# Kernel tuning notes

Measured on AMD Instinct MI355X. Metric: run time of the kernel, lower is better.

Reference implementation:

```python
import jax, jax.numpy as jnp
import numpy as np

D_MODEL = 1024
D_STATE = 64
D_CONV = 4
EXPAND = 2
N_HEADS = 16
D_INNER = D_MODEL * EXPAND            # 2048
HEAD_DIM = D_INNER // N_HEADS         # 128
Z_DIM = D_INNER + 2 * D_STATE * N_HEADS + N_HEADS  # 4112
RMS_EPS = 1.1920928955078125e-07      # torch.finfo(float32).eps (RMSNorm default)


def setup_inputs() -> dict:
    key = jax.random.key(0)
    ks = jax.random.split(key, 6)
    s = 0.02
    u = jax.random.normal(ks[0], (2, 4096, D_MODEL), dtype=jnp.float32)
    W_in = jax.random.normal(ks[1], (D_MODEL, Z_DIM), dtype=jnp.float32) * s
    conv_w = jax.random.normal(ks[2], (D_INNER, D_CONV), dtype=jnp.float32) * s
    conv_b = jnp.zeros((D_INNER,), dtype=jnp.float32)
    delta_param = jnp.zeros((N_HEADS,), dtype=jnp.float32)
    W_gate = jax.random.normal(ks[3], (D_MODEL, D_INNER), dtype=jnp.float32) * s
    norm_w = jnp.ones((D_INNER,), dtype=jnp.float32)
    W_out = jax.random.normal(ks[4], (D_INNER, D_MODEL), dtype=jnp.float32) * s
    return {"u": u, "W_in": W_in, "conv_w": conv_w, "conv_b": conv_b,
            "delta_param": delta_param, "W_gate": W_gate, "norm_w": norm_w, "W_out": W_out}


def _ssm_scan(x, dt, B_mat, C_mat, delta_param):
    # x: (B,L,nh,dh); dt: (B,L,nh); B_mat,C_mat: (B,L,nh,ds)
    delta = jax.nn.softplus(dt + delta_param[None, None, :])
    a_bar = jnp.exp(-delta * jnp.abs(dt))            # (B,L,nh)
    Bsz, L, nh, dh = x.shape
    ds = B_mat.shape[-1]
    h0 = jnp.zeros((Bsz, nh, dh, ds), dtype=x.dtype)

    def step(h, inp):
        a_t, x_t, b_t, c_t = inp                     # (B,nh),(B,nh,dh),(B,nh,ds),(B,nh,ds)
        h = a_t[:, :, None, None] * h + x_t[..., None] * b_t[:, :, None, :]
        y_t = jnp.einsum('bhds,bhs->bhd', h, c_t)
        return h, y_t

    # move time to leading axis for scan
    xs = (jnp.moveaxis(a_bar, 1, 0), jnp.moveaxis(x, 1, 0),
          jnp.moveaxis(B_mat, 1, 0), jnp.moveaxis(C_mat, 1, 0))
    _, ys = jax.lax.scan(step, h0, xs)               # ys: (L,B,nh,dh)
    return jnp.moveaxis(ys, 0, 1)                    # (B,L,nh,dh)


def _forward(u, W_in, conv_w, conv_b, delta_param, W_gate, norm_w, W_out):
    B, L, _ = u.shape
    z = u @ W_in                                      # (B,L,Z_DIM)
    x = z[..., :D_INNER]
    o = D_INNER
    B_mat = z[..., o:o + D_STATE * N_HEADS].reshape(B, L, N_HEADS, D_STATE)
    o += D_STATE * N_HEADS
    C_mat = z[..., o:o + D_STATE * N_HEADS].reshape(B, L, N_HEADS, D_STATE)
    o += D_STATE * N_HEADS
    dt = z[..., o:o + N_HEADS]                        # (B,L,nh)

    # depthwise causal conv1d (kernel size D_CONV, left pad D_CONV-1)
    pad = D_CONV - 1
    xp = jnp.pad(x, ((0, 0), (pad, 0), (0, 0)))       # (B,L+pad,d_inner)
    x_conv = conv_b[None, None, :]
    for k in range(D_CONV):
        x_conv = x_conv + xp[:, k:k + L, :] * conv_w[None, None, :, k]
    x = jax.nn.silu(x_conv)

    x_ssm = x.reshape(B, L, N_HEADS, HEAD_DIM)
    y = _ssm_scan(x_ssm, dt, B_mat, C_mat, delta_param)
    y = y.reshape(B, L, D_INNER)

    gate = jax.nn.sigmoid(u @ W_gate)
    y = gate * y
    # RMSNorm
    y = y * jax.lax.rsqrt(jnp.mean(y * y, axis=-1, keepdims=True) + RMS_EPS) * norm_w
    return y @ W_out


def reference(u, W_in, conv_w, conv_b, delta_param, W_gate, norm_w, W_out):
    return _forward(u, W_in, conv_w, conv_b, delta_param, W_gate, norm_w, W_out)
```

## Files before the change

kernel.cpp:

```cpp
#include <hip/hip_runtime.h>

#define BATCH   2
#define LSEQ    4096
#define DMODEL  1024
#define DINNER  2048
#define NHEADS  16
#define DSTATE  64
#define HEADDIM 128
#define ZDIM    4112
#define BLROWS  (BATCH*LSEQ)
#define QCHUNK  64
#define NCHUNK  (LSEQ/QCHUNK)
#define UPAD    1088
#define GPAD    2112

#define AS1 __attribute__((address_space(1)))
#define AS3 __attribute__((address_space(3)))

typedef __bf16 bf16;
typedef __bf16 bf16x8 __attribute__((ext_vector_type(8)));
typedef __bf16 bf16x4 __attribute__((ext_vector_type(4)));
typedef float  f32x4  __attribute__((ext_vector_type(4)));

__device__ __forceinline__ int lds_elem(int row, int c)
{
    return (row >> 1) * 64 + (row & 1) * 32 + (((c ^ ((row >> 1) & 3)) & 3) << 3);
}

__global__ void cvt_pad_kernel(const float* __restrict__ in, bf16* __restrict__ out)
{
    int gid = blockIdx.x * 256 + threadIdx.x;
    int row = gid >> 8, c4 = (gid & 255) * 4;
    float4 v = *reinterpret_cast<const float4*>(in + (size_t)row * DMODEL + c4);
    bf16x4 o;
    o[0] = (bf16)v.x; o[1] = (bf16)v.y; o[2] = (bf16)v.z; o[3] = (bf16)v.w;
    *reinterpret_cast<bf16x4*>(out + (size_t)row * UPAD + c4) = o;
}

__global__ void transpose_cvt_kernel(const float* __restrict__ src, bf16* __restrict__ dst,
                                     int R, int C, int Cpad, int dstS,
                                     const float* __restrict__ rowscale)
{
    __shared__ float tile[32][33];
    int tx = threadIdx.x;
    int ty = threadIdx.y;
    int c0 = blockIdx.x * 32;
    int r0 = blockIdx.y * 32;
#pragma unroll
    for (int q = 0; q < 4; q++) {
        int r = r0 + ty + q * 8;
        int c = c0 + tx;
        float v = 0.f;
        if (r < R && c < C) v = src[(size_t)r * C + c];
        tile[ty + q * 8][tx] = v;
    }
    __syncthreads();
    float sc = 1.f;
    if (rowscale && (r0 + tx) < R) sc = rowscale[r0 + tx];
#pragma unroll
    for (int q = 0; q < 4; q++) {
        int oc = c0 + ty + q * 8;
        int orr = r0 + tx;
        if (oc < Cpad && orr < R)
            dst[(size_t)oc * dstS + orr] = (bf16)(tile[tx][ty + q * 8] * sc);
    }
}

template<int NSLICE, int KROW, int MODE, int NBN>
__global__ __launch_bounds__(256) void gemm_db3_kernel(
    const bf16* __restrict__ A, const bf16* __restrict__ Bt,
    bf16* __restrict__ z, bf16* __restrict__ g, float* __restrict__ lab,
    const float* __restrict__ dparam, const float* __restrict__ rs, float* __restrict__ c32)
{
    constexpr int SLOTSZ = 256 * 32;
    __shared__ __align__(16) bf16 lds[3 * SLOTSZ];
    const int tid = threadIdx.x;
    const int lane = tid & 63, wid = tid >> 6;
    const int wm = (wid >> 1) * 64, wn = (wid & 1) * 64;
    const int lml = lane & 15, kc = lane >> 4;

    const int bid = blockIdx.x;
    const int xcd = bid & 7;
    const int idx = bid >> 3;
    const int bm = xcd * 8 + (idx & 7);
    const int bn = idx >> 3;

    const bf16* Abase = A + (size_t)(bm * 128) * KROW;
    const bf16* Bbase = Bt + (size_t)(bn * 128) * KROW;

#define STAGE8(pp) do {                                                                  \
    const int _p = (pp); const int _slot = _p % 3; const size_t _ko = (size_t)_p * 32;   \
    _Pragma("unroll") for (int it = 0; it < 4; ++it) {                                   \
        int q = it * 256 + tid;                                                          \
        int o = (q < 512) ? q : q - 512;                                                 \
        int prow = o >> 3, wi = o & 7;                                                   \
        int row = prow * 2 + (wi >> 2), c = (wi & 3) ^ (prow & 3);                       \
        const bf16* _src = ((q < 512) ? Abase : Bbase) + (size_t)row * KROW + _ko + c * 8; \
        int _dst = _slot * SLOTSZ + ((q < 512) ? 0 : 4096) + o * 8;                      \
        __builtin_amdgcn_global_load_lds((const AS1 void*)_src,                          \
            (AS3 void*)(&lds[_dst]), 16, 0, 0);                                          \
    }                                                                                    \
} while (0)

    f32x4 acc[4][4];
#pragma unroll
    for (int i = 0; i < 4; i++)
#pragma unroll
        for (int j = 0; j < 4; j++) acc[i][j] = (f32x4){0.f, 0.f, 0.f, 0.f};

    STAGE8(0); STAGE8(1); STAGE8(2);
    asm volatile("s_waitcnt vmcnt(8)" ::: "memory");
    __builtin_amdgcn_s_barrier();

    for (int p = 0; p < NSLICE; ++p) {
        const bf16* base_ = &lds[(p % 3) * SLOTSZ];
        bf16x8 af[4], bfv[4];
#pragma unroll
        for (int i = 0; i < 4; ++i) {
            int row = wm + i * 16 + lml;
            af[i] = *reinterpret_cast<const bf16x8*>(&base_[lds_elem(row, kc)]);
        }
#pragma unroll
        for (int j = 0; j < 4; ++j) {
            int row = wn + j * 16 + lml;
            bfv[j] = *reinterpret_cast<const bf16x8*>(&base_[4096 + lds_elem(row, kc)]);
        }
        asm volatile("s_waitcnt lgkmcnt(0)" ::: "memory");
        __builtin_amdgcn_sched_barrier(0);
        __builtin_amdgcn_s_barrier();
        if (p + 3 < NSLICE) STAGE8(p + 3);
#pragma unroll
        for (int i = 0; i < 4; ++i)
#pragma unroll
            for (int j = 0; j < 4; ++j)
                acc[i][j] = __builtin_amdgcn_mfma_f32_16x16x32_bf16(af[i], bfv[j], acc[i][j], 0, 0, 0);
        if (p + 1 < NSLICE) {
            if (p + 3 < NSLICE)       { asm volatile("s_waitcnt vmcnt(8)" ::: "memory"); }
            else if (p + 2 < NSLICE)  { asm volatile("s_waitcnt vmcnt(4)" ::: "memory"); }
            else                      { asm volatile("s_waitcnt vmcnt(0)" ::: "memory"); }
            __builtin_amdgcn_s_barrier();
        }
    }
#undef STAGE8

    const int rbase = (lane >> 4) * 4;
#pragma unroll
    for (int i = 0; i < 4; i++) {
#pragma unroll
        for (int j = 0; j < 4; j++) {
            int col = bn * 128 + wn + j * 16 + lml;
            if constexpr (MODE == 0) {
                bool isZ = (col < ZDIM);
                bool isG = (col >= 4224) && (col < 4224 + DINNER);
                bool isDT = (col >= 4096) && (col < ZDIM);
                if (!isZ && !isG) continue;
#pragma unroll
                for (int r = 0; r < 4; r++) {
                    int row = bm * 128 + wm + i * 16 + rbase + r;
                    float v = acc[i][j][r];
                    if (isZ) {
                        z[(size_t)row * ZDIM + col] = (bf16)v;
                        if (isDT) {
                            int h = col - 4096;
                            float v2 = v + dparam[h];
                            float sp = (v2 > 20.f) ? v2 : log1pf(expf(v2));
                            lab[(size_t)row * NHEADS + h] = -sp * fabsf(v);
                        }
                    } else {
                        g[(size_t)row * GPAD + (col - 4224)] = (bf16)v;
                    }
                }
            } else {
                int row0 = bm * 128 + wm + i * 16 + rbase;
                float4 rsv = *reinterpret_cast<const float4*>(rs + row0);
                const float* rp = reinterpret_cast<const float*>(&rsv);
#pragma unroll
                for (int r = 0; r < 4; r++)
                    c32[(size_t)(row0 + r) * 1024 + col] = acc[i][j][r] * rp[r];
            }
        }
    }
}

__global__ __launch_bounds__(256) void chunk_state_kernel(
    const bf16* __restrict__ zz,
    const float* __restrict__ conv_w, const float* __restrict__ conv_b,
    const float* __restrict__ la,
    bf16* __restrict__ S,
    float* __restrict__ Adec)
{
    __shared__ __align__(16) bf16 xt[HEADDIM * QCHUNK];
    __shared__ __align__(16) bf16 bw[DSTATE * QCHUNK];
    __shared__ float Ls[QCHUNK];
    const int blk = blockIdx.x;
    const int h = blk & 15, c = (blk >> 4) & 63, b = blk >> 10;
    const int tid = threadIdx.x, lane = tid & 63, w = tid >> 6;
    const size_t row0 = (size_t)b * LSEQ + (size_t)c * QCHUNK;
    const bf16* zxg = zz + row0 * ZDIM + h * HEADDIM;
    const bf16* Bg  = zz + row0 * ZDIM + DINNER + h * DSTATE;

    const int tg = (tid >> 4) * 4;
    const int dg8 = (tid & 15) * 8;
    float wv[8][4], xa[4][8];
#pragma unroll
    for (int e = 0; e < 8; e++) {
        float4 w4 = *reinterpret_cast<const float4*>(conv_w + (size_t)(h * HEADDIM + dg8 + e) * 4);
        wv[e][0] = w4.x; wv[e][1] = w4.y; wv[e][2] = w4.z; wv[e][3] = w4.w;
        float bb = conv_b[h * HEADDIM + dg8 + e];
#pragma unroll
        for (int tt = 0; tt < 4; tt++) xa[tt][e] = bb;
    }
#pragma unroll
    for (int r = 0; r < 7; r++) {
        int lrow = c * QCHUNK + tg + r - 3;
        if (lrow >= 0) {
            bf16x8 zv = *reinterpret_cast<const bf16x8*>(zxg + (ptrdiff_t)(tg + r - 3) * ZDIM + dg8);
#pragma unroll
            for (int tt = 0; tt < 4; tt++) {
                int k = r - tt;
                if (k >= 0 && k < 4) {
#pragma unroll
                    for (int e = 0; e < 8; e++)
                        xa[tt][e] = fmaf((float)zv[e], wv[e][k], xa[tt][e]);
                }
            }
        }
    }
#pragma unroll
    for (int tt = 0; tt < 4; tt++)
#pragma unroll
        for (int e = 0; e < 8; e++)
            xa[tt][e] = xa[tt][e] / (1.f + expf(-xa[tt][e]));

    const int t = tid >> 2, sseg = (tid & 3) * 16;
    bf16x8 br[2];
#pragma unroll
    for (int q = 0; q < 2; q++)
        br[q] = *reinterpret_cast<const bf16x8*>(Bg + (size_t)t * ZDIM + sseg + q * 8);

    if (w == 0) {
        float v = la[(row0 + lane) * NHEADS + h];
#pragma unroll
        for (int off = 1; off < 64; off <<= 1) { float o = __shfl_up(v, off); if (lane >= off) v += o; }
        Ls[lane] = v;
        if (lane == 63) Adec[((size_t)b * NHEADS + h) * NCHUNK + c] = __expf(v);
    }
    __syncthreads();
    const float wt = __expf(Ls[QCHUNK - 1] - Ls[t]);
#pragma unroll
    for (int tt = 0; tt < 4; tt++) {
        int t2 = tg + tt;
#pragma unroll
        for (int e = 0; e < 8; e++) {
            int d = dg8 + e;
            xt[d * 64 + (((t2 >> 3) ^ (d & 7)) << 3) + (t2 & 7)] = (bf16)xa[tt][e];
        }
    }
    const int tb = t >> 3, ti = t & 7;
#pragma unroll
    for (int q = 0; q < 2; q++)
#pragma unroll
        for (int j = 0; j < 8; j++) {
            int s = sseg + q * 8 + j;
            bw[s * 64 + ((tb ^ (s & 7)) << 3) + ti] = (bf16)((float)br[q][j] * wt);
        }
    __syncthreads();

    f32x4 acc[2][4];
#pragma unroll
    for (int i = 0; i < 2; i++)
#pragma unroll
        for (int j = 0; j < 4; j++) acc[i][j] = (f32x4){0.f, 0.f, 0.f, 0.f};
#pragma unroll
    for (int kk = 0; kk < 2; kk++) {
        const int kb = kk * 4 + (lane >> 4);
        bf16x8 af[2], bf2[4];
#pragma unroll
        for (int i = 0; i < 2; i++) {
            int d = w * 32 + i * 16 + (lane & 15);
            af[i] = *reinterpret_cast<const bf16x8*>(&xt[d * 64 + ((kb ^ (d & 7)) << 3)]);
        }
#pragma unroll
        for (int j = 0; j < 4; j++) {
            int s = j * 16 + (lane & 15);
            bf2[j] = *reinterpret_cast<const bf16x8*>(&bw[s * 64 + ((kb ^ (s & 7)) << 3)]);
        }
#pragma unroll
        for (int i = 0; i < 2; i++)
#pragma unroll
            for (int j = 0; j < 4; j++)
                acc[i][j] = __builtin_amdgcn_mfma_f32_16x16x32_bf16(af[i], bf2[j], acc[i][j], 0, 0, 0);
    }
    bf16* Sg = S + ((size_t)(b * NCHUNK + c) * NHEADS + h) * (HEADDIM * DSTATE);
    const int rr = (lane >> 4) * 4, ccol = lane & 15;
#pragma unroll
    for (int i = 0; i < 2; i++)
#pragma unroll
        for (int j = 0; j < 4; j++)
#pragma unroll
            for (int r = 0; r < 4; r++)
                Sg[(w * 32 + i * 16 + rr + r) * 64 + j * 16 + ccol] = (bf16)acc[i][j][r];
}

__global__ void chunk_carry_kernel(bf16* S, const float* __restrict__ A)
{
    int gid = blockIdx.x * 256 + threadIdx.x;
    if (gid >= BATCH * NHEADS * HEADDIM * DSTATE) return;
    int es = gid & (HEADDIM * DSTATE - 1);
    int h  = (gid >> 13) & (NHEADS - 1);
    int b  = gid >> 17;
    const float* Ab = A + ((size_t)b * NHEADS + h) * NCHUNK;
    float hstate = 0.f;
    size_t stride = (size_t)NHEADS * HEADDIM * DSTATE;
    bf16* p = S + ((size_t)b * NCHUNK * NHEADS + h) * (HEADDIM * DSTATE) + es;
    for (int c = 0; c < NCHUNK; ++c) {
        float sv = (float)*p;
        *p = (bf16)hstate;
        hstate = fmaf(Ab[c], hstate, sv);
        p += stride;
    }
}

__global__ __launch_bounds__(256) void chunk_y_kernel(
    bf16* __restrict__ gv,
    const bf16* __restrict__ zz,
    const float* __restrict__ conv_w, const float* __restrict__ conv_b,
    const float* __restrict__ la,
    const bf16* __restrict__ H,
    float* __restrict__ psum)
{
    __shared__ __align__(16) bf16 bc[QCHUNK * 128];
    __shared__ __align__(16) bf16 xt[HEADDIM * QCHUNK];
    __shared__ __align__(16) bf16 hl[HEADDIM * DSTATE];
    __shared__ float Ls[QCHUNK];
    __shared__ float wsum[4][QCHUNK];
    const int blk = blockIdx.x;
    const int h = blk & 15, c = (blk >> 4) & 63, b = blk >> 10;
    const int tid = threadIdx.x, lane = tid & 63, w = tid >> 6;
    const size_t row0 = (size_t)b * LSEQ + (size_t)c * QCHUNK;
    bf16* gg = gv + row0 * GPAD + h * HEADDIM;
    const bf16* zxg = zz + row0 * ZDIM + h * HEADDIM;
    const bf16* Bg = zz + row0 * ZDIM + DINNER + h * DSTATE;
    const bf16* Cg = Bg + NHEADS * DSTATE;
    const bf16* Hg = H + ((size_t)(b * NCHUNK + c) * NHEADS + h) * (HEADDIM * DSTATE);

#pragma unroll
    for (int it = 0; it < 2; it++) {
        int idx = it * 256 + tid;
        int row = idx >> 3, p = idx & 7;
        int sc = (p ^ (row & 7)) << 3;
        __builtin_amdgcn_global_load_lds((const AS1 void*)(Bg + (size_t)row * ZDIM + sc),
                                         (AS3 void*)(&bc[idx * 8]), 16, 0, 0);
        __builtin_amdgcn_global_load_lds((const AS1 void*)(Cg + (size_t)row * ZDIM + sc),
                                         (AS3 void*)(&bc[4096 + idx * 8]), 16, 0, 0);
    }
#pragma unroll
    for (int it = 0; it < 4; it++) {
        int idx = it * 256 + tid;
        int d = idx >> 3, p = idx & 7;
        __builtin_amdgcn_global_load_lds((const AS1 void*)(Hg + d * 64 + ((p ^ (d & 7)) << 3)),
                                         (AS3 void*)(&hl[idx * 8]), 16, 0, 0);
    }

    const int tg = (tid >> 4) * 4;
    const int dg8 = (tid & 15) * 8;
    float wv[8][4], xa[4][8];
#pragma unroll
    for (int e = 0; e < 8; e++) {
        float4 w4 = *reinterpret_cast<const float4*>(conv_w + (size_t)(h * HEADDIM + dg8 + e) * 4);
        wv[e][0] = w4.x; wv[e][1] = w4.y; wv[e][2] = w4.z; wv[e][3] = w4.w;
        float bb = conv_b[h * HEADDIM + dg8 + e];
#pragma unroll
        for (int tt = 0; tt < 4; tt++) xa[tt][e] = bb;
    }
#pragma unroll
    for (int r = 0; r < 7; r++) {
        int lrow = c * QCHUNK + tg + r - 3;
        if (lrow >= 0) {
            bf16x8 zv = *reinterpret_cast<const bf16x8*>(zxg + (ptrdiff_t)(tg + r - 3) * ZDIM + dg8);
#pragma unroll
            for (int tt = 0; tt < 4; tt++) {
                int k = r - tt;
                if (k >= 0 && k < 4) {
#pragma unroll
                    for (int e = 0; e < 8; e++)
                        xa[tt][e] = fmaf((float)zv[e], wv[e][k], xa[tt][e]);
                }
            }
        }
    }
#pragma unroll
    for (int tt = 0; tt < 4; tt++)
#pragma unroll
        for (int e = 0; e < 8; e++)
            xa[tt][e] = xa[tt][e] / (1.f + expf(-xa[tt][e]));

    const int t = tid >> 2, sseg = (tid & 3) * 16;
    if (w == 0) {
        float v = la[(row0 + lane) * NHEADS + h];
#pragma unroll
        for (int off = 1; off < 64; off <<= 1) { float o = __shfl_up(v, off); if (lane >= off) v += o; }
        Ls[lane] = v;
    }
    __syncthreads();

#pragma unroll
    for (int tt = 0; tt < 4; tt++) {
        int t2 = tg + tt;
#pragma unroll
        for (int e = 0; e < 8; e++) {
            int d = dg8 + e;
            xt[d * 64 + (((t2 >> 3) ^ (d & 7)) << 3) + (t2 & 7)] = (bf16)xa[tt][e];
        }
    }

    f32x4 g[4];
#pragma unroll
    for (int j = 0; j < 4; j++) g[j] = (f32x4){0.f, 0.f, 0.f, 0.f};
#pragma unroll
    for (int kk = 0; kk < 2; kk++) {
        const int kb = kk * 4 + (lane >> 4);
        const int tA = w * 16 + (lane & 15);
        bf16x8 ca = *reinterpret_cast<const bf16x8*>(&bc[4096 + tA * 64 + ((kb ^ (tA & 7)) << 3)]);
#pragma unroll
        for (int j = 0; j < 4; j++) {
            int tB = j * 16 + (lane & 15);
            bf16x8 bb = *reinterpret_cast<const bf16x8*>(&bc[tB * 64 + ((kb ^ (tB & 7)) << 3)]);
            g[j] = __builtin_amdgcn_mfma_f32_16x16x32_bf16(ca, bb, g[j], 0, 0, 0);
        }
    }
    bf16x8 cr[2];
#pragma unroll
    for (int q = 0; q < 2; q++) {
        int sblk = (sseg >> 3) + q;
        cr[q] = *reinterpret_cast<const bf16x8*>(&bc[4096 + t * 64 + ((sblk ^ (t & 7)) << 3)]);
    }
    const float pscale = __expf(Ls[t]);
    __syncthreads();

    {
        const int tpbase = lane & 15;
        const int tgbase = w * 16 + (lane >> 4) * 4;
        float lst[4];
#pragma unroll
        for (int r = 0; r < 4; r++) lst[r] = Ls[tgbase + r];
#pragma unroll
        for (int j = 0; j < 4; j++) {
            int tp = j * 16 + tpbase;
            float lstp = Ls[tp];
#pragma unroll
            for (int r = 0; r < 4; r++) {
                int tg2 = tgbase + r;
                float mg = (tp <= tg2) ? g[j][r] * __expf(lst[r] - lstp) : 0.f;
                bc[tg2 * 128 + (((tp >> 3) ^ (tg2 & 7)) << 3) + (tp & 7)] = (bf16)mg;
            }
        }
    }
#pragma unroll
    for (int q = 0; q < 2; q++) {
        int sblk = (sseg >> 3) + q;
        bf16x8 o;
#pragma unroll
        for (int j = 0; j < 8; j++) o[j] = (bf16)((float)cr[q][j] * pscale);
        *reinterpret_cast<bf16x8*>(&bc[t * 128 + ((8 + (sblk ^ (t & 7))) << 3)]) = o;
    }
    __syncthreads();

    f32x4 acc[2][4];
#pragma unroll
    for (int i = 0; i < 2; i++)
#pragma unroll
        for (int j = 0; j < 4; j++) acc[i][j] = (f32x4){0.f, 0.f, 0.f, 0.f};
#pragma unroll
    for (int kk = 0; kk < 4; kk++) {
        const int kb = kk * 4 + (lane >> 4);
        bf16x8 af[2];
#pragma unroll
        for (int i = 0; i < 2; i++) {
            int d = w * 32 + i * 16 + (lane & 15);
            if (kk < 2)
                af[i] = *reinterpret_cast<const bf16x8*>(&xt[d * 64 + ((kb ^ (d & 7)) << 3)]);
            else
                af[i] = *reinterpret_cast<const bf16x8*>(&hl[d * 64 + (((kb - 8) ^ (d & 7)) << 3)]);
        }
#pragma unroll
        for (int j = 0; j < 4; j++) {
            int tt = j * 16 + (lane & 15);
            bf16x8 b2 = *reinterpret_cast<const bf16x8*>(&bc[tt * 128 + ((kb ^ (tt & 7)) << 3)]);
#pragma unroll
            for (int i = 0; i < 2; i++)
                acc[i][j] = __builtin_amdgcn_mfma_f32_16x16x32_bf16(af[i], b2, acc[i][j], 0, 0, 0);
        }
    }

    float ps[4] = {0.f, 0.f, 0.f, 0.f};
#pragma unroll
    for (int i = 0; i < 2; i++)
#pragma unroll
        for (int j = 0; j < 4; j++) {
            int d0 = w * 32 + i * 16 + (lane >> 4) * 4;
            int tt = j * 16 + (lane & 15);
            bf16x4 gt = *reinterpret_cast<const bf16x4*>(gg + (size_t)tt * GPAD + d0);
            bf16x4 o;
#pragma unroll
            for (int r = 0; r < 4; r++) {
                float gf = (float)gt[r];
                float vv = acc[i][j][r] / (1.f + expf(-gf));
                o[r] = (bf16)vv;
                ps[j] = fmaf(vv, vv, ps[j]);
            }
            *reinterpret_cast<bf16x4*>(gg + (size_t)tt * GPAD + d0) = o;
        }
#pragma unroll
    for (int j = 0; j < 4; j++) {
        ps[j] += __shfl_xor(ps[j], 16);
        ps[j] += __shfl_xor(ps[j], 32);
    }
    if ((lane >> 4) == 0) {
#pragma unroll
        for (int j = 0; j < 4; j++) wsum[w][j * 16 + (lane & 15)] = ps[j];
    }
    __syncthreads();
    if (tid < QCHUNK) {
        float tot = wsum[0][tid] + wsum[1][tid] + wsum[2][tid] + wsum[3][tid];
        psum[(row0 + tid) * NHEADS + h] = tot;
    }
}

__global__ void rowscale_kernel(const float* __restrict__ psum, float* __restrict__ rs)
{
    int r = blockIdx.x * 256 + threadIdx.x;
    if (r >= BLROWS) return;
    float s = 0.f;
#pragma unroll
    for (int h = 0; h < NHEADS; h++) s += psum[(size_t)r * NHEADS + h];
    rs[r] = rsqrtf(s * (1.0f / DINNER) + 1.1920928955078125e-07f);
}

extern "C" void kernel_launch(void* const* d_in, const int* in_sizes, int n_in,
                              void* d_out, int out_size, void* d_ws, size_t ws_size,
                              hipStream_t stream)
{
    const float* u      = (const float*)d_in[0];
    const float* W_in   = (const float*)d_in[1];
    const float* conv_w = (const float*)d_in[2];
    const float* conv_b = (const float*)d_in[3];
    const float* dparam = (const float*)d_in[4];
    const float* W_gate = (const float*)d_in[5];
    const float* norm_w = (const float*)d_in[6];
    const float* W_out  = (const float*)d_in[7];
    float* out = (float*)d_out;

    char* ws = (char*)d_ws;
    size_t off = 0;
    auto alloc = [&](size_t bytes) {
        void* p = ws + off;
        off += (bytes + 255) & ~(size_t)255;
        return p;
    };
    bf16*  u_bf  = (bf16*) alloc((size_t)BLROWS * UPAD * 2);
    bf16*  Wt_f  = (bf16*) alloc((size_t)6400 * UPAD * 2);
    bf16*  Wt_o  = (bf16*) alloc((size_t)DMODEL * GPAD * 2);
    bf16*  z     = (bf16*) alloc((size_t)BLROWS * ZDIM * 2);
    bf16*  g     = (bf16*) alloc((size_t)BLROWS * GPAD * 2);
    float* lab   = (float*)alloc((size_t)BLROWS * NHEADS * 4);
    bf16*  S     = (bf16*) alloc((size_t)BATCH * NCHUNK * NHEADS * HEADDIM * DSTATE * 2);
    float* Adec  = (float*)alloc((size_t)BATCH * NHEADS * NCHUNK * 4);
    float* psum  = (float*)alloc((size_t)BLROWS * NHEADS * 4);
    float* rs    = (float*)alloc((size_t)BLROWS * 4);
    (void)ws_size; (void)in_sizes; (void)n_in; (void)out_size;

    dim3 tb(32, 8);
    cvt_pad_kernel<<<BLROWS, 256, 0, stream>>>(u, u_bf);
    transpose_cvt_kernel<<<dim3(4224 / 32, DMODEL / 32), tb, 0, stream>>>(W_in, Wt_f, DMODEL, ZDIM, 4224, UPAD, nullptr);
    transpose_cvt_kernel<<<dim3(2176 / 32, DMODEL / 32), tb, 0, stream>>>(W_gate, Wt_f + (size_t)4224 * UPAD, DMODEL, DINNER, 2176, UPAD, nullptr);
    transpose_cvt_kernel<<<dim3(DMODEL / 32, DINNER / 32), tb, 0, stream>>>(W_out, Wt_o, DINNER, DMODEL, DMODEL, GPAD, norm_w);

    gemm_db3_kernel<32, UPAD, 0, 50><<<64 * 50, 256, 0, stream>>>(
        u_bf, Wt_f, z, g, lab, dparam, nullptr, nullptr);

    chunk_state_kernel<<<BATCH * NCHUNK * NHEADS, 256, 0, stream>>>(z, conv_w, conv_b, lab, S, Adec);
    chunk_carry_kernel<<<(BATCH * NHEADS * HEADDIM * DSTATE) / 256, 256, 0, stream>>>(S, Adec);
    chunk_y_kernel<<<BATCH * NCHUNK * NHEADS, 256, 0, stream>>>(g, z, conv_w, conv_b, lab, S, psum);

    rowscale_kernel<<<(BLROWS + 255) / 256, 256, 0, stream>>>(psum, rs);

    gemm_db3_kernel<64, GPAD, 1, 8><<<64 * 8, 256, 0, stream>>>(
        g, Wt_o, nullptr, nullptr, nullptr, nullptr, rs, out);
}
```

Measured before the change: 321.7 us.

## Merge prep kernels, pack gate columns densely, fold rowscale into output GEMM

Merges the u conversion and the three weight transposes into a single prep launch that dispatches on block index. The gate columns are packed directly after the z columns (at 4112 instead of 4224), so the fused input GEMM needs 49 column tiles instead of 50. The separate rowscale kernel is removed: each block of the output GEMM sums the per-head partials for its 128 rows into shared memory. This saves several launches and one tile column of GEMM work, at the cost of redundant rowscale computation in every column block and a boundary tile that now writes both z and g.

```diff
diff --git a/kernel.cpp b/kernel.cpp
--- a/kernel.cpp
+++ b/kernel.cpp
@@ -13,6 +13,8 @@
 #define NCHUNK  (LSEQ/QCHUNK)
 #define UPAD    1088
 #define GPAD    2112
+#define NGATE0  4112
+#define NFUSE2  6272
 
 #define AS1 __attribute__((address_space(1)))
 #define AS3 __attribute__((address_space(3)))
@@ -27,25 +29,14 @@
     return (row >> 1) * 64 + (row & 1) * 32 + (((c ^ ((row >> 1) & 3)) & 3) << 3);
 }
 
-__global__ void cvt_pad_kernel(const float* __restrict__ in, bf16* __restrict__ out)
-{
-    int gid = blockIdx.x * 256 + threadIdx.x;
-    int row = gid >> 8, c4 = (gid & 255) * 4;
-    float4 v = *reinterpret_cast<const float4*>(in + (size_t)row * DMODEL + c4);
-    bf16x4 o;
-    o[0] = (bf16)v.x; o[1] = (bf16)v.y; o[2] = (bf16)v.z; o[3] = (bf16)v.w;
-    *reinterpret_cast<bf16x4*>(out + (size_t)row * UPAD + c4) = o;
-}
-
-__global__ void transpose_cvt_kernel(const float* __restrict__ src, bf16* __restrict__ dst,
-                                     int R, int C, int Cpad, int dstS,
-                                     const float* __restrict__ rowscale)
+__device__ __forceinline__ void do_transpose(const float* __restrict__ src, bf16* __restrict__ dst,
+                                             int R, int C, int Cpad, int dstS,
+                                             const float* __restrict__ rowscale,
+                                             int bx, int by, int tid)
 {
     __shared__ float tile[32][33];
-    int tx = threadIdx.x;
-    int ty = threadIdx.y;
-    int c0 = blockIdx.x * 32;
-    int r0 = blockIdx.y * 32;
+    int tx = tid & 31, ty = tid >> 5;
+    int c0 = bx * 32, r0 = by * 32;
 #pragma unroll
     for (int q = 0; q < 4; q++) {
         int r = r0 + ty + q * 8;
@@ -66,14 +57,45 @@
     }
 }
 
+#define PREP_CVT   8192
+#define PREP_WIN   (PREP_CVT + 129 * 32)
+#define PREP_WG    (PREP_WIN + 68 * 32)
+#define PREP_WO    (PREP_WG + 32 * 64)
+__global__ __launch_bounds__(256) void prep_kernel(
+    const float* __restrict__ u, const float* __restrict__ W_in,
+    const float* __restrict__ W_gate, const float* __restrict__ W_out,
+    const float* __restrict__ norm_w,
+    bf16* __restrict__ u_bf, bf16* __restrict__ Wt_f, bf16* __restrict__ Wt_o)
+{
+    int b = blockIdx.x, tid = threadIdx.x;
+    if (b < PREP_CVT) {
+        int row = b, c4 = tid * 4;
+        float4 v = *reinterpret_cast<const float4*>(u + (size_t)row * DMODEL + c4);
+        bf16x4 o;
+        o[0] = (bf16)v.x; o[1] = (bf16)v.y; o[2] = (bf16)v.z; o[3] = (bf16)v.w;
+        *reinterpret_cast<bf16x4*>(u_bf + (size_t)row * UPAD + c4) = o;
+    } else if (b < PREP_WIN) {
+        int t = b - PREP_CVT;
+        do_transpose(W_in, Wt_f, DMODEL, ZDIM, NGATE0, UPAD, nullptr, t % 129, t / 129, tid);
+    } else if (b < PREP_WG) {
+        int t = b - PREP_WIN;
+        do_transpose(W_gate, Wt_f + (size_t)NGATE0 * UPAD, DMODEL, DINNER, 2160, UPAD, nullptr,
+                     t % 68, t / 68, tid);
+    } else {
+        int t = b - PREP_WG;
+        do_transpose(W_out, Wt_o, DINNER, DMODEL, DMODEL, GPAD, norm_w, t & 31, t >> 5, tid);
+    }
+}
+
 template<int NSLICE, int KROW, int MODE, int NBN>
 __global__ __launch_bounds__(256) void gemm_db3_kernel(
     const bf16* __restrict__ A, const bf16* __restrict__ Bt,
     bf16* __restrict__ z, bf16* __restrict__ g, float* __restrict__ lab,
-    const float* __restrict__ dparam, const float* __restrict__ rs, float* __restrict__ c32)
+    const float* __restrict__ dparam, const float* __restrict__ psum, float* __restrict__ c32)
 {
     constexpr int SLOTSZ = 256 * 32;
     __shared__ __align__(16) bf16 lds[3 * SLOTSZ];
+    __shared__ float srs[128];
     const int tid = threadIdx.x;
     const int lane = tid & 63, wid = tid >> 6;
     const int wm = (wid >> 1) * 64, wn = (wid & 1) * 64;
@@ -102,6 +124,16 @@
     }                                                                                    \
 } while (0)
 
+    if constexpr (MODE == 1) {
+        if (tid < 128) {
+            int row = bm * 128 + tid;
+            float s = 0.f;
+#pragma unroll
+            for (int h = 0; h < NHEADS; h++) s += psum[(size_t)row * NHEADS + h];
+            srs[tid] = rsqrtf(s * (1.0f / DINNER) + 1.1920928955078125e-07f);
+        }
+    }
+
     f32x4 acc[4][4];
 #pragma unroll
     for (int i = 0; i < 4; i++)
@@ -151,7 +183,7 @@
             int col = bn * 128 + wn + j * 16 + lml;
             if constexpr (MODE == 0) {
                 bool isZ = (col < ZDIM);
-                bool isG = (col >= 4224) && (col < 4224 + DINNER);
+                bool isG = (col >= NGATE0) && (col < NGATE0 + DINNER);
                 bool isDT = (col >= 4096) && (col < ZDIM);
                 if (!isZ && !isG) continue;
 #pragma unroll
@@ -166,17 +198,17 @@
                             float sp = (v2 > 20.f) ? v2 : log1pf(expf(v2));
                             lab[(size_t)row * NHEADS + h] = -sp * fabsf(v);
                         }
-                    } else {
-                        g[(size_t)row * GPAD + (col - 4224)] = (bf16)v;
+                    }
+                    if (isG) {
+                        g[(size_t)row * GPAD + (col - NGATE0)] = (bf16)v;
                     }
                 }
             } else {
                 int row0 = bm * 128 + wm + i * 16 + rbase;
-                float4 rsv = *reinterpret_cast<const float4*>(rs + row0);
-                const float* rp = reinterpret_cast<const float*>(&rsv);
+                int l0 = wm + i * 16 + rbase;
 #pragma unroll
                 for (int r = 0; r < 4; r++)
-                    c32[(size_t)(row0 + r) * 1024 + col] = acc[i][j][r] * rp[r];
+                    c32[(size_t)(row0 + r) * 1024 + col] = acc[i][j][r] * srs[l0 + r];
             }
         }
     }
@@ -527,16 +559,6 @@
     }
 }
 
-__global__ void rowscale_kernel(const float* __restrict__ psum, float* __restrict__ rs)
-{
-    int r = blockIdx.x * 256 + threadIdx.x;
-    if (r >= BLROWS) return;
-    float s = 0.f;
-#pragma unroll
-    for (int h = 0; h < NHEADS; h++) s += psum[(size_t)r * NHEADS + h];
-    rs[r] = rsqrtf(s * (1.0f / DINNER) + 1.1920928955078125e-07f);
-}
-
 extern "C" void kernel_launch(void* const* d_in, const int* in_sizes, int n_in,
                               void* d_out, int out_size, void* d_ws, size_t ws_size,
                               hipStream_t stream)
@@ -559,7 +581,7 @@
         return p;
     };
     bf16*  u_bf  = (bf16*) alloc((size_t)BLROWS * UPAD * 2);
-    bf16*  Wt_f  = (bf16*) alloc((size_t)6400 * UPAD * 2);
+    bf16*  Wt_f  = (bf16*) alloc((size_t)6288 * UPAD * 2);
     bf16*  Wt_o  = (bf16*) alloc((size_t)DMODEL * GPAD * 2);
     bf16*  z     = (bf16*) alloc((size_t)BLROWS * ZDIM * 2);
     bf16*  g     = (bf16*) alloc((size_t)BLROWS * GPAD * 2);
@@ -567,24 +589,17 @@
     bf16*  S     = (bf16*) alloc((size_t)BATCH * NCHUNK * NHEADS * HEADDIM * DSTATE * 2);
     float* Adec  = (float*)alloc((size_t)BATCH * NHEADS * NCHUNK * 4);
     float* psum  = (float*)alloc((size_t)BLROWS * NHEADS * 4);
-    float* rs    = (float*)alloc((size_t)BLROWS * 4);
     (void)ws_size; (void)in_sizes; (void)n_in; (void)out_size;
 
-    dim3 tb(32, 8);
-    cvt_pad_kernel<<<BLROWS, 256, 0, stream>>>(u, u_bf);
-    transpose_cvt_kernel<<<dim3(4224 / 32, DMODEL / 32), tb, 0, stream>>>(W_in, Wt_f, DMODEL, ZDIM, 4224, UPAD, nullptr);
-    transpose_cvt_kernel<<<dim3(2176 / 32, DMODEL / 32), tb, 0, stream>>>(W_gate, Wt_f + (size_t)4224 * UPAD, DMODEL, DINNER, 2176, UPAD, nullptr);
-    transpose_cvt_kernel<<<dim3(DMODEL / 32, DINNER / 32), tb, 0, stream>>>(W_out, Wt_o, DINNER, DMODEL, DMODEL, GPAD, norm_w);
-
-    gemm_db3_kernel<32, UPAD, 0, 50><<<64 * 50, 256, 0, stream>>>(
+    prep_kernel<<<PREP_WO, 256, 0, stream>>>(u, W_in, W_gate, W_out, norm_w, u_bf, Wt_f, Wt_o);
+
+    gemm_db3_kernel<32, UPAD, 0, 49><<<64 * 49, 256, 0, stream>>>(
         u_bf, Wt_f, z, g, lab, dparam, nullptr, nullptr);
 
     chunk_state_kernel<<<BATCH * NCHUNK * NHEADS, 256, 0, stream>>>(z, conv_w, conv_b, lab, S, Adec);
     chunk_carry_kernel<<<(BATCH * NHEADS * HEADDIM * DSTATE) / 256, 256, 0, stream>>>(S, Adec);
     chunk_y_kernel<<<BATCH * NCHUNK * NHEADS, 256, 0, stream>>>(g, z, conv_w, conv_b, lab, S, psum);
 
-    rowscale_kernel<<<(BLROWS + 255) / 256, 256, 0, stream>>>(psum, rs);
-
     gemm_db3_kernel<64, GPAD, 1, 8><<<64 * 8, 256, 0, stream>>>(
-        g, Wt_o, nullptr, nullptr, nullptr, nullptr, rs, out);
-}
+        g, Wt_o, nullptr, nullptr, nullptr, nullptr, psum, out);
+}
```

Result: faster. 313.4 us (-2.6%).
